# Kernel tuning notes

Measured on AMD Instinct MI355X. Metric: run time of the kernel, lower is better.

The kernel has to match this reference:

```python
import jax, jax.numpy as jnp
import numpy as np
from jax import lax

KS = 21      # ksize
SCALE = 4    # downscale stride


def _conv(x, w, b=None, padding='SAME'):
    # x: NCHW, w: OIHW
    y = lax.conv_general_dilated(x, w, (1, 1), padding,
                                 dimension_numbers=('NCHW', 'OIHW', 'NCHW'))
    if b is not None:
        y = y + b[None, :, None, None]
    return y


def _deg_kernel_net(z, conv0_w, conv0_b, res_w1, res_b1, res_w2, res_b2, last_w, last_b):
    # conv3x3 -> nb EDSR ResBlocks (conv-relu-conv + residual) -> conv1x1 to ksize^2
    h = _conv(z, conv0_w, conv0_b)
    for i in range(res_w1.shape[0]):  # fixed small layer count
        r = _conv(jax.nn.relu(_conv(h, res_w1[i], res_b1[i])), res_w2[i], res_b2[i])
        h = h + r
    return _conv(h, last_w, last_b)  # (B, ksize^2, H', W')


def setup_inputs() -> dict:
    key = jax.random.key(0)
    ks = jax.random.split(key, 10)
    B, C, H, W = 8, 3, 256, 256
    nf, nb, k2 = 64, 8, KS * KS
    s = 0.05  # keep activations tame through 8 residual blocks
    return {
        'x': jax.random.normal(ks[0], (B, C, H, W), jnp.float32),
        'z': jax.random.normal(ks[1], (B, C, H // SCALE, W // SCALE), jnp.float32),
        'conv0_w': jax.random.normal(ks[2], (nf, C, 3, 3), jnp.float32) * s,
        'conv0_b': jax.random.normal(ks[3], (nf,), jnp.float32) * s,
        'res_w1': jax.random.normal(ks[4], (nb, nf, nf, 3, 3), jnp.float32) * s,
        'res_b1': jax.random.normal(ks[5], (nb, nf), jnp.float32) * s,
        'res_w2': jax.random.normal(ks[6], (nb, nf, nf, 3, 3), jnp.float32) * s,
        'res_b2': jax.random.normal(ks[7], (nb, nf), jnp.float32) * s,
        'last_w': jax.random.normal(ks[8], (k2, nf, 1, 1), jnp.float32) * s,
        'last_b': jax.random.normal(ks[9], (k2,), jnp.float32) * s,
    }


def reference(x, z, conv0_w, conv0_b, res_w1, res_b1, res_w2, res_b2, last_w, last_b):
    B, C, H, W = x.shape
    hz, wz = z.shape[2], z.shape[3]
    k2 = KS * KS

    # spatially-varying kernel, normalized over the ksize^2 taps
    kernel = _deg_kernel_net(z, conv0_w, conv0_b, res_w1, res_b1,
                             res_w2, res_b2, last_w, last_b)
    kernel = kernel.reshape(B, 1, k2, hz, wz)
    kernel = kernel / (kernel.sum(axis=2, keepdims=True) + 1e-8)

    # reflection pad then unfold (im2col) with stride = scale
    p = KS // 2
    xp = jnp.pad(x.reshape(B * C, 1, H, W), ((0, 0), (0, 0), (p, p), (p, p)),
                 mode='reflect')
    patches = lax.conv_general_dilated_patches(
        xp, (KS, KS), (SCALE, SCALE), 'VALID',
        dimension_numbers=('NCHW', 'OIHW', 'NCHW'))  # (B*C, k2, hz, wz)
    patches = patches.reshape(B, C, k2, hz, wz)

    out = (patches * kernel).sum(axis=2)  # (B, C, hz, wz)
    return out, kernel.reshape(B, k2, hz, wz)
```

## Files before the change

### kernel.cpp

```cpp
#include <hip/hip_runtime.h>


#define NB 8
#define NF 64
#define SP 4096
#define PS 66
#define PS2 4356
#define K2 441
#define K2P 448
#define RES_WSTRIDE (64*64*9)
#define WF_RES 36864
#define WF_C0  1792
#define WTA_N  28672

typedef double vdbl4 __attribute__((ext_vector_type(4)));

#define T_AI 0
#define T_AK 64
#define T_BK 128
#define T_BJ 192
#define T_DI 256
#define T_DJ 512

__global__ void probe_mfma(double* __restrict__ probe)
{
    int l = threadIdx.x;
    vdbl4 z = {0.0, 0.0, 0.0, 0.0};
    vdbl4 r1 = __builtin_amdgcn_mfma_f64_16x16x4f64((double)l, 1.0, z, 0, 0, 0);
    vdbl4 r2 = __builtin_amdgcn_mfma_f64_16x16x4f64(1.0, (double)l, z, 0, 0, 0);
#pragma unroll
    for (int r = 0; r < 4; ++r) {
        probe[r * 64 + l]       = r1[r];
        probe[256 + r * 64 + l] = r2[r];
    }
}

__global__ void decode_probe(const double* __restrict__ probe, int* __restrict__ tabs)
{
    int t = threadIdx.x;
    const double* d1 = probe;
    const double* d2 = probe + 256;
    bool fA = ((((int)d1[0]) & 3) == 0);
    bool fB = ((((int)d2[0]) & 3) == 0);
    int v1 = (int)d1[t], v2 = (int)d2[t];
    tabs[T_DI + t] = fA ? (v1 - 96) >> 2 : (v1 - 6) >> 4;
    tabs[T_DJ + t] = fB ? (v2 - 96) >> 2 : (v2 - 6) >> 4;
    if (t < 64) {
        tabs[T_AI + t] = fA ? (t & 15) : (t >> 2);
        tabs[T_AK + t] = fA ? (t >> 4) : (t & 3);
        tabs[T_BK + t] = fB ? (t >> 4) : (t & 3);
        tabs[T_BJ + t] = fB ? (t & 15) : (t >> 2);
    }
}

__global__ void prep_zpad(const float* __restrict__ z, double* __restrict__ zp)
{
    int i = blockIdx.x * blockDim.x + threadIdx.x;
    if (i >= NB * 3 * SP) return;
    int bc = i >> 12, p = i & 4095, y = p >> 6, x = p & 63;
    zp[(size_t)(bc * PS + y + 1) * PS + x + 1] = (double)z[i];
}

__global__ void prep_convw_frag(const float* __restrict__ src, double* __restrict__ dst,
                                const int* __restrict__ tabs,
                                int CIN, int nlayer, int wstride)
{
    int i = blockIdx.x * blockDim.x + threadIdx.x;
    int NS = (CIN * 9 + 3) / 4;
    int M  = NS * 256;
    if (i >= nlayer * M) return;
    int li  = i / M;
    int rem = i - li * M;
    int t   = rem >> 8;
    int j   = rem & 255;
    int mt  = j >> 6;
    int l   = j & 63;
    int kg  = t * 4 + tabs[T_AK + l];
    int oc  = mt * 16 + tabs[T_AI + l];
    int c   = kg / 9;
    int tap = kg - c * 9;
    dst[i] = (kg < CIN * 9) ? (double)src[li * wstride + (oc * CIN + c) * 9 + tap] : 0.0;
}

__global__ void prep_bias_frag(const float* __restrict__ src, double* __restrict__ dst,
                               const int* __restrict__ tabs, int nlayer)
{
    int i = blockIdx.x * blockDim.x + threadIdx.x;
    if (i >= nlayer * 1024) return;
    int li  = i >> 10;
    int j   = i & 1023;
    int mtr = j >> 6;
    int l   = j & 63;
    int mt  = mtr >> 2, r = mtr & 3;
    dst[i] = (double)src[li * 64 + mt * 16 + tabs[T_DI + r * 64 + l]];
}

__global__ void prep_lastwa(const float* __restrict__ lw, const float* __restrict__ lb,
                            const int* __restrict__ tabs,
                            double* __restrict__ wta, double* __restrict__ lbp)
{
    int i = blockIdx.x * blockDim.x + threadIdx.x;
    if (i < WTA_N) {
        int kk = i / (28 * 64);
        int rem = i - kk * (28 * 64);
        int mt = rem >> 6;
        int l  = rem & 63;
        int c  = kk * 4 + tabs[T_AK + l];
        int T  = mt * 16 + tabs[T_AI + l];
        wta[i] = (T < K2) ? (double)lw[T * 64 + c] : 0.0;
    }
    if (i < K2P) lbp[i] = (i < K2) ? (double)lb[i] : 0.0;
}

__global__ void prep_wsum(const float* __restrict__ lw, const float* __restrict__ lb,
                          double* __restrict__ wsum)
{
    int c = threadIdx.x;
    if (c < 64) {
        double s = 0.0;
        for (int t = 0; t < K2; ++t) s += (double)lw[t * 64 + c];
        wsum[c] = s;
    }
    if (c == 64) {
        double s = 0.0;
        for (int t = 0; t < K2; ++t) s += (double)lb[t];
        wsum[64] = s;
    }
}

template<int CIN, bool RELU, bool RESADD>
__global__ __launch_bounds__(256, 2)
void conv3x3_mfma(const double* __restrict__ in, const double* __restrict__ WF,
                  const double* __restrict__ BF, const int* __restrict__ tabs,
                  const double* __restrict__ res, double* __restrict__ out)
{
    constexpr int KT = CIN * 9;
    constexpr int NS = (KT + 3) / 4;
    constexpr int G  = (NS + 8) / 9;

    const int bid = blockIdx.x;
    const int b   = bid & 7;
    const int y0  = bid >> 3;
    const int tid = threadIdx.x;
    const int w   = tid >> 6;
    const int l   = tid & 63;
    const int mi  = w >> 1, ni = w & 1;
    const int mt0 = mi * 2, nt0 = ni * 2;

    const int kB = tabs[T_BK + l];
    const int jB = tabs[T_BJ + l];

    int offp[9];
#pragma unroll
    for (int s = 0; s < 9; ++s) {
        int kg  = s * 4 + kB;
        int off = 0;
        if (KT >= 36 || kg < KT) {
            int c   = kg / 9;
            int tap = kg - c * 9;
            int dy  = tap / 3, dx = tap - dy * 3;
            off = c * PS2 + dy * PS + dx;
        }
        offp[s] = off + jB + nt0 * 16;
    }

    const double* bbase = in + (size_t)b * CIN * PS2 + (size_t)y0 * PS;

    vdbl4 acc[2][2];
#pragma unroll
    for (int mt = 0; mt < 2; ++mt)
#pragma unroll
        for (int r = 0; r < 4; ++r) {
            double bv = BF[((mt0 + mt) * 4 + r) * 64 + l];
            acc[mt][0][r] = bv;
            acc[mt][1][r] = bv;
        }

    double aS[3][2], bS[3][2];
    auto ldA = [&](int t, int slot) {
        const double* p = WF + (size_t)t * 256 + l;
        aS[slot][0] = p[mt0 * 64];
        aS[slot][1] = p[(mt0 + 1) * 64];
    };
    auto ldB = [&](size_t cg, int s, int slot) {
        const double* p = bbase + cg + offp[s];
        bS[slot][0] = p[0];
        bS[slot][1] = p[16];
    };
    auto step = [&](int slot) {
        acc[0][0] = __builtin_amdgcn_mfma_f64_16x16x4f64(aS[slot][0], bS[slot][0], acc[0][0], 0, 0, 0);
        acc[0][1] = __builtin_amdgcn_mfma_f64_16x16x4f64(aS[slot][0], bS[slot][1], acc[0][1], 0, 0, 0);
        acc[1][0] = __builtin_amdgcn_mfma_f64_16x16x4f64(aS[slot][1], bS[slot][0], acc[1][0], 0, 0, 0);
        acc[1][1] = __builtin_amdgcn_mfma_f64_16x16x4f64(aS[slot][1], bS[slot][1], acc[1][1], 0, 0, 0);
    };

    ldA(0, 0); ldB(0, 0, 0);
    ldA(1, 1); ldB(0, 1, 1);

    for (int g = 0; g < G; ++g) {
        const size_t cg = (size_t)g * 4 * PS2;
#pragma unroll
        for (int s = 0; s < 9; ++s) {
            const int t = g * 9 + s;
            if (KT % 36 != 0 && t >= NS) break;
            const int tp = t + 2;
            if (tp < NS) {
                const int    ps  = (s + 2 < 9) ? s + 2 : s - 7;
                const size_t pcg = (s + 2 < 9) ? cg : cg + 4 * PS2;
                ldA(tp, (s + 2) % 3);
                ldB(pcg, ps, (s + 2) % 3);
            }
            step(s % 3);
        }
    }

    int iD[4], jD[4];
#pragma unroll
    for (int r = 0; r < 4; ++r) {
        iD[r] = tabs[T_DI + r * 64 + l];
        jD[r] = tabs[T_DJ + r * 64 + l];
    }
#pragma unroll
    for (int mt = 0; mt < 2; ++mt)
#pragma unroll
        for (int nt = 0; nt < 2; ++nt)
#pragma unroll
            for (int r = 0; r < 4; ++r) {
                int oc = (mt0 + mt) * 16 + iD[r];
                int x  = (nt0 + nt) * 16 + jD[r];
                size_t idx = (size_t)(b * NF + oc) * PS2 + (size_t)(y0 + 1) * PS + x + 1;
                double val = acc[mt][nt][r];
                if (RELU)   val = fmax(val, 0.0);
                if (RESADD) val += res[idx];
                out[idx] = val;
            }
}

__global__ __launch_bounds__(256, 2)
void lastconv_mfma(const double* __restrict__ hp, const double* __restrict__ wta,
                   const double* __restrict__ lbp, const int* __restrict__ tabs,
                   const double* __restrict__ inv_sums, float* __restrict__ kraw)
{
    const int bid = blockIdx.x;
    const int b   = bid / 224;
    const int rem = bid - b * 224;
    const int tg  = rem >> 5;
    const int pc  = rem & 31;
    const int tid = threadIdx.x;
    const int w   = tid >> 6;
    const int l   = tid & 63;
    const int mt  = tg * 4 + w;

    const int kB = tabs[T_BK + l];
    const int jB = tabs[T_BJ + l];
    int iD[4], jD[4];
#pragma unroll
    for (int r = 0; r < 4; ++r) {
        iD[r] = tabs[T_DI + r * 64 + l];
        jD[r] = tabs[T_DJ + r * 64 + l];
    }

    double avs[16];
#pragma unroll
    for (int kk = 0; kk < 16; ++kk)
        avs[kk] = wta[((size_t)kk * 28 + mt) * 64 + l];

    double bias[4];
#pragma unroll
    for (int r = 0; r < 4; ++r)
        bias[r] = lbp[mt * 16 + iD[r]];

    const double* hb = hp + (size_t)b * NF * PS2;
    float* kb = kraw + (size_t)b * K2 * SP;

    for (int q = 0; q < 2; ++q) {
        const int P0  = pc * 128 + q * 64;
        const int row = P0 >> 6;
        const double* hrow = hb + (size_t)(row + 1) * PS + 1 + jB;

        const double* isrow = inv_sums + (size_t)b * SP + P0;
        double isv[4][4];
#pragma unroll
        for (int j = 0; j < 4; ++j)
#pragma unroll
            for (int r = 0; r < 4; ++r)
                isv[j][r] = isrow[j * 16 + jD[r]];

        vdbl4 acc[4];
#pragma unroll
        for (int j = 0; j < 4; ++j)
#pragma unroll
            for (int r = 0; r < 4; ++r)
                acc[j][r] = bias[r];

        double bc[4], bn[4];
#pragma unroll
        for (int j = 0; j < 4; ++j)
            bc[j] = hrow[(size_t)kB * PS2 + j * 16];

        for (int kk = 0; kk < 16; ++kk) {
            if (kk < 15) {
                const double* np = hrow + (size_t)((kk + 1) * 4 + kB) * PS2;
#pragma unroll
                for (int j = 0; j < 4; ++j) bn[j] = np[j * 16];
            }
#pragma unroll
            for (int j = 0; j < 4; ++j)
                acc[j] = __builtin_amdgcn_mfma_f64_16x16x4f64(avs[kk], bc[j], acc[j], 0, 0, 0);
#pragma unroll
            for (int j = 0; j < 4; ++j) bc[j] = bn[j];
        }

#pragma unroll
        for (int r = 0; r < 4; ++r) {
            int T = mt * 16 + iD[r];
            if (T < K2) {
                float* p = kb + (size_t)T * SP + P0;
                p[jD[r]]      = (float)(acc[0][r] * isv[0][r]);
                p[16 + jD[r]] = (float)(acc[1][r] * isv[1][r]);
                p[32 + jD[r]] = (float)(acc[2][r] * isv[2][r]);
                p[48 + jD[r]] = (float)(acc[3][r] * isv[3][r]);
            }
        }
    }
}

__global__ __launch_bounds__(256)
void sums_kernel(const double* __restrict__ hp, const double* __restrict__ wsum,
                 double* __restrict__ inv_sums)
{
    int i = blockIdx.x * 256 + threadIdx.x;
    int b = i >> 12, p = i & 4095;
    int y = p >> 6, x = p & 63;
    const double* hb = hp + (size_t)b * NF * PS2 + (size_t)(y + 1) * PS + 1 + x;
    double s = wsum[64];
    for (int c = 0; c < 64; ++c) s += hb[(size_t)c * PS2] * wsum[c];
    inv_sums[b * SP + p] = 1.0 / (s + 1e-8);
}

__global__ __launch_bounds__(256)
void apply_kernel(const float* __restrict__ x, const float* __restrict__ kout,
                  float* __restrict__ out)
{
    const int bid  = blockIdx.x;
    const int g    = bid & 3;
    const int tile = (bid >> 2) & 15;
    const int b    = bid >> 6;
    const int i0   = (tile >> 2) << 4;
    const int j0   = (tile & 3) << 4;
    const int tid  = threadIdx.x;
    const int ti   = tid >> 4, tj = tid & 15;

    __shared__ float s_x[3][81][84];

    for (int e = tid; e < 3 * 81 * 84; e += 256) {
        int c   = e / 6804;
        int rem = e - c * 6804;
        int u   = rem / 84;
        int v   = rem - u * 84;
        int gr  = i0 * 4 + u - 10;
        int gc  = j0 * 4 + v - 10;
        gr = gr < 0 ? -gr : (gr > 255 ? 510 - gr : gr);
        gc = gc < 0 ? -gc : (gc > 255 ? 510 - gc : gc);
        int vp = (v & 3) * 21 + (v >> 2);
        s_x[c][u][vp] = x[((b * 3 + c) * 256 + gr) * 256 + gc];
    }
    __syncthreads();

    const int p = (i0 + ti) * 64 + (j0 + tj);

    float o0 = 0.f, o1 = 0.f, o2 = 0.f;
    const int t0 = g * 111;
    const int t1 = (t0 + 111 < K2) ? t0 + 111 : K2;
    for (int t = t0; t < t1; ++t) {
        int ty = t / 21, tx = t - ty * 21;
        float kn = kout[(size_t)(b * K2 + t) * SP + p];
        int u  = ti * 4 + ty;
        int vp = (tx & 3) * 21 + tj + (tx >> 2);
        o0 = fmaf(s_x[0][u][vp], kn, o0);
        o1 = fmaf(s_x[1][u][vp], kn, o1);
        o2 = fmaf(s_x[2][u][vp], kn, o2);
    }
    atomicAdd(&out[(b * 3 + 0) * SP + p], o0);
    atomicAdd(&out[(b * 3 + 1) * SP + p], o1);
    atomicAdd(&out[(b * 3 + 2) * SP + p], o2);
}

extern "C" void kernel_launch(void* const* d_in, const int* in_sizes, int n_in,
                              void* d_out, int out_size, void* d_ws, size_t ws_size,
                              hipStream_t stream)
{
    (void)in_sizes; (void)n_in; (void)out_size; (void)ws_size;

    const float* x = (const float*)d_in[0];
    const float* z = (const float*)d_in[1];

    float* out  = (float*)d_out;
    float* kout = (float*)d_out + NB * 3 * SP;

    double* wd    = (double*)d_ws;
    double* probe = wd;
    int*    tabs  = (int*)(wd + 512);
    double* wf0   = wd + 1024;
    double* wf1   = wf0 + WF_C0;
    double* wf2   = wf1 + 8 * WF_RES;
    double* bf0   = wf2 + 8 * WF_RES;
    double* bf1   = bf0 + 1024;
    double* bf2   = bf1 + 8 * 1024;
    double* wta   = bf2 + 8 * 1024;
    double* lbp   = wta + WTA_N;
    double* wsum  = lbp + K2P;
    double* zp    = wsum + 72;
    double* hp    = zp + NB * 3 * PS2;
    double* tp    = hp + NB * NF * PS2;
    double* sums  = tp;

    hipMemsetAsync(zp, 0, (size_t)NB * 3 * PS2 * sizeof(double), stream);
    hipMemsetAsync(hp, 0, (size_t)NB * NF * PS2 * sizeof(double), stream);
    hipMemsetAsync(tp, 0, (size_t)NB * NF * PS2 * sizeof(double), stream);
    hipMemsetAsync(out, 0, NB * 3 * SP * sizeof(float), stream);

    probe_mfma<<<1, 64, 0, stream>>>(probe);
    decode_probe<<<1, 256, 0, stream>>>(probe, tabs);

    prep_zpad<<<(NB * 3 * SP + 255) / 256, 256, 0, stream>>>(z, zp);
    prep_convw_frag<<<(WF_C0 + 255) / 256, 256, 0, stream>>>(
        (const float*)d_in[2], wf0, tabs, 3, 1, 0);
    prep_convw_frag<<<(8 * WF_RES + 255) / 256, 256, 0, stream>>>(
        (const float*)d_in[4], wf1, tabs, 64, 8, RES_WSTRIDE);
    prep_convw_frag<<<(8 * WF_RES + 255) / 256, 256, 0, stream>>>(
        (const float*)d_in[6], wf2, tabs, 64, 8, RES_WSTRIDE);
    prep_bias_frag<<<(1024 + 255) / 256, 256, 0, stream>>>(
        (const float*)d_in[3], bf0, tabs, 1);
    prep_bias_frag<<<(8 * 1024 + 255) / 256, 256, 0, stream>>>(
        (const float*)d_in[5], bf1, tabs, 8);
    prep_bias_frag<<<(8 * 1024 + 255) / 256, 256, 0, stream>>>(
        (const float*)d_in[7], bf2, tabs, 8);
    prep_lastwa<<<(WTA_N + 255) / 256, 256, 0, stream>>>(
        (const float*)d_in[8], (const float*)d_in[9], tabs, wta, lbp);
    prep_wsum<<<1, 128, 0, stream>>>(
        (const float*)d_in[8], (const float*)d_in[9], wsum);

    conv3x3_mfma<3,  false, false><<<512, 256, 0, stream>>>(zp, wf0, bf0, tabs, nullptr, hp);
    for (int i = 0; i < 8; ++i) {
        conv3x3_mfma<64, true,  false><<<512, 256, 0, stream>>>(
            hp, wf1 + i * WF_RES, bf1 + i * 1024, tabs, nullptr, tp);
        conv3x3_mfma<64, false, true ><<<512, 256, 0, stream>>>(
            tp, wf2 + i * WF_RES, bf2 + i * 1024, tabs, hp, hp);
    }
    sums_kernel<<<128, 256, 0, stream>>>(hp, wsum, sums);
    lastconv_mfma<<<1792, 256, 0, stream>>>(hp, wta, lbp, tabs, sums, kout);
    apply_kernel<<<512, 256, 0, stream>>>(x, kout, out);
}
```

Baseline: 908.5 us.

## Restructure apply kernel to per-row blocks with direct global reads and LDS reduction

Rewrites the final spatially-varying convolution so each block handles one output row of 64 pixels, with four tap chunks reduced in shared memory instead of through global atomics. The reflection-padded input tile is no longer staged in LDS; each thread reads its input pixels directly from global memory (through cache), computing reflected indices per tap. Because outputs are written directly, the memset of the output buffer is dropped. This trades LDS staging for strided uncoalesced global loads (stride 4 across lanes), which may put more pressure on the cache.

```diff
diff --git a/kernel.cpp b/kernel.cpp
--- a/kernel.cpp
+++ b/kernel.cpp
@@ -342,48 +342,48 @@
 void apply_kernel(const float* __restrict__ x, const float* __restrict__ kout,
                   float* __restrict__ out)
 {
-    const int bid  = blockIdx.x;
-    const int g    = bid & 3;
-    const int tile = (bid >> 2) & 15;
-    const int b    = bid >> 6;
-    const int i0   = (tile >> 2) << 4;
-    const int j0   = (tile & 3) << 4;
-    const int tid  = threadIdx.x;
-    const int ti   = tid >> 4, tj = tid & 15;
-
-    __shared__ float s_x[3][81][84];
-
-    for (int e = tid; e < 3 * 81 * 84; e += 256) {
-        int c   = e / 6804;
-        int rem = e - c * 6804;
-        int u   = rem / 84;
-        int v   = rem - u * 84;
-        int gr  = i0 * 4 + u - 10;
-        int gc  = j0 * 4 + v - 10;
-        gr = gr < 0 ? -gr : (gr > 255 ? 510 - gr : gr);
-        gc = gc < 0 ? -gc : (gc > 255 ? 510 - gc : gc);
-        int vp = (v & 3) * 21 + (v >> 2);
-        s_x[c][u][vp] = x[((b * 3 + c) * 256 + gr) * 256 + gc];
-    }
-    __syncthreads();
-
-    const int p = (i0 + ti) * 64 + (j0 + tj);
+    const int bid   = blockIdx.x;
+    const int b     = bid >> 6;
+    const int row   = bid & 63;
+    const int tid   = threadIdx.x;
+    const int chunk = tid >> 6;
+    const int px    = tid & 63;
+    const int p     = row * 64 + px;
+
+    const float* xb = x + (size_t)b * 3 * 65536;
+    const float* kb = kout + (size_t)b * K2 * SP + p;
 
     float o0 = 0.f, o1 = 0.f, o2 = 0.f;
-    const int t0 = g * 111;
+    const int t0 = chunk * 111;
     const int t1 = (t0 + 111 < K2) ? t0 + 111 : K2;
     for (int t = t0; t < t1; ++t) {
         int ty = t / 21, tx = t - ty * 21;
-        float kn = kout[(size_t)(b * K2 + t) * SP + p];
-        int u  = ti * 4 + ty;
-        int vp = (tx & 3) * 21 + tj + (tx >> 2);
-        o0 = fmaf(s_x[0][u][vp], kn, o0);
-        o1 = fmaf(s_x[1][u][vp], kn, o1);
-        o2 = fmaf(s_x[2][u][vp], kn, o2);
-    }
-    atomicAdd(&out[(b * 3 + 0) * SP + p], o0);
-    atomicAdd(&out[(b * 3 + 1) * SP + p], o1);
-    atomicAdd(&out[(b * 3 + 2) * SP + p], o2);
+        float kn = kb[(size_t)t * SP];
+        int gr = row * 4 + ty - 10;
+        int gc = px * 4 + tx - 10;
+        gr = gr < 0 ? -gr : (gr > 255 ? 510 - gr : gr);
+        gc = gc < 0 ? -gc : (gc > 255 ? 510 - gc : gc);
+        const float* xp = xb + gr * 256 + gc;
+        o0 = fmaf(xp[0],       kn, o0);
+        o1 = fmaf(xp[65536],   kn, o1);
+        o2 = fmaf(xp[131072],  kn, o2);
+    }
+
+    __shared__ float red[3][4][64];
+    if (chunk > 0) {
+        red[0][chunk][px] = o0;
+        red[1][chunk][px] = o1;
+        red[2][chunk][px] = o2;
+    }
+    __syncthreads();
+    if (chunk == 0) {
+        o0 += red[0][1][px] + red[0][2][px] + red[0][3][px];
+        o1 += red[1][1][px] + red[1][2][px] + red[1][3][px];
+        o2 += red[2][1][px] + red[2][2][px] + red[2][3][px];
+        out[(b * 3 + 0) * SP + p] = o0;
+        out[(b * 3 + 1) * SP + p] = o1;
+        out[(b * 3 + 2) * SP + p] = o2;
+    }
 }
 
 extern "C" void kernel_launch(void* const* d_in, const int* in_sizes, int n_in,
@@ -418,7 +418,6 @@
     hipMemsetAsync(zp, 0, (size_t)NB * 3 * PS2 * sizeof(double), stream);
     hipMemsetAsync(hp, 0, (size_t)NB * NF * PS2 * sizeof(double), stream);
     hipMemsetAsync(tp, 0, (size_t)NB * NF * PS2 * sizeof(double), stream);
-    hipMemsetAsync(out, 0, NB * 3 * SP * sizeof(float), stream);
 
     probe_mfma<<<1, 64, 0, stream>>>(probe);
     decode_probe<<<1, 256, 0, stream>>>(probe, tabs);
```

After: 895.6 us. No clear change (-1.4%).
